# Kernel optimization log

Hardware: AMD Instinct MI355X
Metric: run time of the kernel (lower is better)

Reference implementation:

```python
import jax, jax.numpy as jnp
import numpy as np

N = 200000
E = 6400000
NEG_SLOPE = 0.01  # nn.LeakyReLU default

def _leaky(x):
    return jnp.where(x >= 0, x, NEG_SLOPE * x)

def gcn_conv(x, edge_index, W, b, n):
    # PyG GCNConv: add self-loops, symmetric degree norm, linear, scatter-add, bias
    src, dst = edge_index[0], edge_index[1]
    loops = jnp.arange(n, dtype=src.dtype)
    src = jnp.concatenate([src, loops])
    dst = jnp.concatenate([dst, loops])
    deg = jax.ops.segment_sum(jnp.ones_like(dst, dtype=x.dtype), dst, num_segments=n)
    dinv = jnp.where(deg > 0, jax.lax.rsqrt(deg), 0.0)
    norm = dinv[src] * dinv[dst]                  # [E+N]
    h = x @ W.T                                   # [N,50] linear (no bias yet)
    msg = h[src] * norm[:, None]                  # gather + scale
    out = jax.ops.segment_sum(msg, dst, num_segments=n)  # scatter-add to targets
    return out + b

def setup_inputs() -> dict:
    key = jax.random.key(0)
    ks = jax.random.split(key, 20)
    def w(k, o, i):
        return jax.random.normal(k, (o, i), dtype=jnp.float32) * (1.0 / np.sqrt(i))
    def bvec(k, o):
        return jax.random.normal(k, (o,), dtype=jnp.float32) * 0.01
    inp = {
        'x': jax.random.normal(ks[0], (N, 150), dtype=jnp.float32),
        'edge_index': jax.random.randint(ks[1], (2, E), 0, N, dtype=jnp.int64 if jax.config.jax_enable_x64 else jnp.int32),
        'epsilon': jax.random.normal(ks[2], (N, 10), dtype=jnp.float32),
        'Wg': w(ks[3], 50, 50), 'bg': bvec(ks[4], 50),
        'We1': w(ks[5], 40, 50), 'be1': bvec(ks[6], 40),
        'We2': w(ks[7], 30, 40), 'be2': bvec(ks[8], 30),
        'We3': w(ks[9], 20, 30), 'be3': bvec(ks[10], 20),
        'Wfc': w(ks[11], 10, 10), 'bfc': bvec(ks[12], 10),
        'Wd1': w(ks[13], 20, 10), 'bd1': bvec(ks[14], 20),
        'Wd2': w(ks[15], 40, 20), 'bd2': bvec(ks[16], 40),
        'Wd3': w(ks[17], 50, 40), 'bd3': bvec(ks[18], 50),
    }
    return inp

def reference(x, edge_index, epsilon, Wg, bg, We1, be1, We2, be2, We3, be3,
              Wfc, bfc, Wd1, bd1, Wd2, bd2, Wd3, bd3):
    x1 = x[:, 100:]                                   # [N,50]
    h = gcn_conv(x1, edge_index, Wg, bg, x.shape[0])  # [N,50]
    # encoder
    e = _leaky(h @ We1.T + be1)
    e = _leaky(e @ We2.T + be2)
    e = e @ We3.T + be3                               # [N,20]
    mu, log_var = e[:, :10], e[:, 10:]
    # reparameterization: mu + eps * sqrt(exp(log_var))
    z1 = mu + epsilon * jnp.exp(0.5 * log_var)
    z = jax.nn.relu(z1 @ Wfc.T + bfc)                 # FC
    # decoder
    d = _leaky(z @ Wd1.T + bd1)
    d = _leaky(d @ Wd2.T + bd2)
    mu_prime = jax.nn.sigmoid(d @ Wd3.T + bd3)        # [N,50]
    return (mu_prime, mu, log_var, z)
```

## Files before the change

kernel.cpp:

```cpp
#include <hip/hip_runtime.h>


#define NEG 0.01f
#define GS 64
#define ELLS 64
#define NB 16
#define SPILL_CAP 65536

#define DET_ES (1024 * 1024)
#define IS64_THRESH (DET_ES / 2)

#define META_INTS 1024

typedef int vint2 __attribute__((ext_vector_type(2)));

static __device__ __forceinline__ float bf2f(unsigned short u) {
    return __uint_as_float(((unsigned)u) << 16);
}
static __device__ __forceinline__ float leaky(float a) { return (a >= 0.f) ? a : NEG * a; }

__global__ void k_zero(int* __restrict__ indeg, int* __restrict__ flag,
                       int* __restrict__ meta, int n) {
    int i = blockIdx.x * 256 + threadIdx.x;
    if (i < n) indeg[i] = 0;
    if (blockIdx.x == 0) {
        for (int j = threadIdx.x; j < META_INTS; j += 256) meta[j] = 0;
        if (threadIdx.x == 0) { flag[0] = 0; flag[1] = 0; flag[2] = 0; }
    }
}

__global__ void k_detect(const unsigned* __restrict__ x, long xwords,
                         const unsigned* __restrict__ ei, long epairs,
                         int* __restrict__ flag) {
    int gw = (blockIdx.x * 256 + threadIdx.x) >> 6;
    int lane = threadIdx.x & 63;
    int side = gw >> 10;
    int ch = gw & 1023;
    int c = 0;
    if (side == 0) {
        long step = xwords >> 10;
        long base = (long)ch * step;
        if (base + 1024 > xwords) base = xwords > 1024 ? xwords - 1024 : 0;
#pragma unroll
        for (int t = 0; t < 16; t++) {
            long idx = base + t * 64 + lane;
            if (idx < xwords) {
                unsigned w = x[idx];
                if (((w >> 23) & 0xFFu) == 0xFFu || ((w >> 7) & 0xFFu) == 0xFFu) c++;
            }
        }
        for (int k = 32; k; k >>= 1) c += __shfl_xor(c, k);
        if (lane == 0 && c) atomicAdd(&flag[0], c);
    } else {
        long step = epairs >> 10;
        long base = (long)ch * step;
        if (base + 1024 > epairs) base = epairs > 1024 ? epairs - 1024 : 0;
#pragma unroll
        for (int t = 0; t < 16; t++) {
            long idx = base + t * 64 + lane;
            if (idx < epairs && ei[2 * idx + 1] == 0u) c++;
        }
        for (int k = 32; k; k >>= 1) c += __shfl_xor(c, k);
        if (lane == 0 && c) atomicAdd(&flag[1], c);
    }
}

__global__ __launch_bounds__(256) void k_hist(const int* __restrict__ ei,
                                              const int* __restrict__ flag,
                                              int* __restrict__ meta, int E, int N) {
    __shared__ int lh[NB];
    if (threadIdx.x < NB) lh[threadIdx.x] = 0;
    __syncthreads();
    bool is64 = flag[1] > IS64_THRESH;
    unsigned usw = ((unsigned)N + NB - 1) / NB;
    const long stride = 1024L * 256;
    if (is64) {
        const int2* p = (const int2*)ei;
        for (long e = (long)blockIdx.x * 256 + threadIdx.x; e < E; e += stride) {
            int d = p[E + e].x;
            if ((unsigned)d < (unsigned)N) atomicAdd(&lh[(unsigned)d / usw], 1);
        }
    } else {
        for (long e = (long)blockIdx.x * 256 + threadIdx.x; e < E; e += stride) {
            int d = ei[E + e];
            if ((unsigned)d < (unsigned)N) atomicAdd(&lh[(unsigned)d / usw], 1);
        }
    }
    __syncthreads();
    if (threadIdx.x < NB && lh[threadIdx.x]) atomicAdd(&meta[threadIdx.x * 16], lh[threadIdx.x]);
}

__global__ void k_scan(int* __restrict__ meta) {
    if (threadIdx.x == 0) {
        int acc = 0;
        for (int k = 0; k < NB; k++) {
            int c = meta[k * 16];
            meta[256 + k] = acc;
            meta[512 + k * 16] = acc;
            acc += c;
            meta[288 + k] = acc;
        }
    }
}

__global__ __launch_bounds__(256) void k_part(const int* __restrict__ ei,
                                              const int* __restrict__ flag,
                                              int* __restrict__ meta,
                                              int2* __restrict__ bucket, int E, int N) {
    __shared__ int2 buf[NB][512];
    __shared__ int lcnt[NB];
    __shared__ int lbase;
    if (threadIdx.x < NB) lcnt[threadIdx.x] = 0;
    __syncthreads();
    bool is64 = flag[1] > IS64_THRESH;
    unsigned usw = ((unsigned)N + NB - 1) / NB;
    int nsteps = (E + 2048 * 256 - 1) / (2048 * 256);
    for (int step = 0; step < nsteps; step++) {
        long e = (long)(step * 2048 + blockIdx.x) * 256 + threadIdx.x;
        int b = -1;
        int2 sd;
        if (e < E) {
            int src, d;
            if (is64) {
                const int2* p = (const int2*)ei;
                src = p[e].x;
                d = p[E + e].x;
            } else {
                src = ei[e];
                d = ei[E + e];
            }
            if ((unsigned)d < (unsigned)N) {
                b = (int)((unsigned)d / usw);
                sd = make_int2(src, d);
            }
        }
        if (b >= 0) {
            int p = atomicAdd(&lcnt[b], 1);
            buf[b][p] = sd;
        }
        __syncthreads();
        for (int k = 0; k < NB; k++) {
            int cnt = lcnt[k];
            if (cnt >= 256) {
                if (threadIdx.x == 0) lbase = atomicAdd(&meta[512 + k * 16], 256);
                __syncthreads();
                bucket[lbase + threadIdx.x] = buf[k][threadIdx.x];
                int rem = cnt - 256;
                int2 r;
                if (threadIdx.x < rem) r = buf[k][256 + threadIdx.x];
                __syncthreads();
                if (threadIdx.x < rem) buf[k][threadIdx.x] = r;
                if (threadIdx.x == 0) lcnt[k] = rem;
                __syncthreads();
            }
        }
    }
    for (int k = 0; k < NB; k++) {
        int cnt = lcnt[k];
        if (cnt > 0) {
            if (threadIdx.x == 0) lbase = atomicAdd(&meta[512 + k * 16], cnt);
            __syncthreads();
            if (threadIdx.x < cnt) bucket[lbase + threadIdx.x] = buf[k][threadIdx.x];
            __syncthreads();
        }
    }
}

__global__ __launch_bounds__(256) void k_build2(const int2* __restrict__ bucket,
                                                const int* __restrict__ meta,
                                                int* __restrict__ indeg,
                                                int* __restrict__ ebuf,
                                                int2* __restrict__ spill,
                                                int* __restrict__ flag, int N, int pass) {
    int s = pass * 8 + (blockIdx.x & 7);
    int q = blockIdx.x >> 3;
    int lo = meta[256 + s];
    int hi = meta[288 + s];
    for (int idx = lo + q * 256 + threadIdx.x; idx < hi; idx += 512 * 256) {
        vint2 t = __builtin_nontemporal_load((const vint2*)&bucket[idx]);
        int src = t.x;
        int d = t.y;
        if ((unsigned)src >= (unsigned)N) continue;
        int c = atomicAdd(&indeg[d], 1);
        if (c < ELLS) {
            ebuf[(size_t)d * ELLS + c] = src;
        } else {
            int o = atomicAdd(&flag[2], 1);
            if (o < SPILL_CAP) spill[o] = make_int2(src, d);
        }
    }
}

__global__ void k_dinv(const int* __restrict__ indeg, float* __restrict__ dinv, int n) {
    int i = blockIdx.x * 256 + threadIdx.x;
    if (i < n) dinv[i] = rsqrtf(1.0f + (float)indeg[i]);
}

struct CW {
    const void* src[16];
    int off[16];
    int n[16];
};
__global__ void k_convw(CW cw, float* __restrict__ dst, const int* __restrict__ flag) {
    int b = blockIdx.x;
    bool isf = flag[0] > 64;
    const float* sf = (const float*)cw.src[b];
    const unsigned short* sh = (const unsigned short*)cw.src[b];
    float* d = dst + cw.off[b];
    int n = cw.n[b];
    for (int i = threadIdx.x; i < n; i += 256) d[i] = isf ? sf[i] : bf2f(sh[i]);
}

#define O_WG 0
#define O_BG 2500
#define O_WE1 2550
#define O_BE1 4550
#define O_WE2 4590
#define O_BE2 5790
#define O_WE3 5820
#define O_BE3 6420
#define O_WFC 6440
#define O_BFC 6540
#define O_WD1 6550
#define O_BD1 6750
#define O_WD2 6770
#define O_BD2 7570
#define O_WD3 7610
#define O_BD3 9610
#define W_TOT 9660

__global__ __launch_bounds__(256) void k_g(const void* __restrict__ xv,
                                           const float* __restrict__ W,
                                           const float* __restrict__ dinv,
                                           const int* __restrict__ flag,
                                           float* __restrict__ g, int n) {
    int i = blockIdx.x * 256 + threadIdx.x;
    if (i >= n) return;
    bool isf = flag[0] > 64;
    float xr[50];
    if (isf) {
        const float* p = (const float*)xv + (size_t)i * 150 + 100;
#pragma unroll
        for (int k = 0; k < 50; k++) xr[k] = p[k];
    } else {
        const unsigned short* p = (const unsigned short*)xv + (size_t)i * 150 + 100;
#pragma unroll
        for (int k = 0; k < 50; k++) xr[k] = bf2f(p[k]);
    }
    const float* Wg = W + O_WG;
    float di = dinv[i];
    float* gr = g + (size_t)i * GS;
#pragma unroll
    for (int f = 0; f < 50; f += 2) {
        float a0 = 0.f, a1 = 0.f;
#pragma unroll
        for (int p = 0; p < 50; p++) {
            a0 += Wg[f * 50 + p] * xr[p];
            a1 += Wg[(f + 1) * 50 + p] * xr[p];
        }
        gr[f] = a0 * di;
        gr[f + 1] = a1 * di;
    }
}

__global__ __launch_bounds__(256) void k_gather(const float* __restrict__ g,
                                                const int* __restrict__ indeg,
                                                const int* __restrict__ ebuf,
                                                const float* __restrict__ dinv,
                                                const float* __restrict__ W,
                                                float* __restrict__ h1, int n) {
    int wid = threadIdx.x >> 6;
    int lane = threadIdx.x & 63;
    int i = blockIdx.x * 4 + wid;
    if (i >= n) return;
    int fc = lane < 50 ? lane : 49;
    int cnt = indeg[i];
    if (cnt > ELLS) cnt = ELLS;
    float di = dinv[i];
    int ev = (lane < cnt) ? ebuf[(size_t)i * ELLS + lane] : 0;
    float a0 = g[(size_t)i * GS + fc];
    float a1 = 0.f, a2 = 0.f, a3 = 0.f, a4 = 0.f, a5 = 0.f, a6 = 0.f, a7 = 0.f;
    int m = 0;
    for (; m + 7 < cnt; m += 8) {
        int j0 = __shfl(ev, m);
        int j1 = __shfl(ev, m + 1);
        int j2 = __shfl(ev, m + 2);
        int j3 = __shfl(ev, m + 3);
        int j4 = __shfl(ev, m + 4);
        int j5 = __shfl(ev, m + 5);
        int j6 = __shfl(ev, m + 6);
        int j7 = __shfl(ev, m + 7);
        a0 += g[(size_t)j0 * GS + fc];
        a1 += g[(size_t)j1 * GS + fc];
        a2 += g[(size_t)j2 * GS + fc];
        a3 += g[(size_t)j3 * GS + fc];
        a4 += g[(size_t)j4 * GS + fc];
        a5 += g[(size_t)j5 * GS + fc];
        a6 += g[(size_t)j6 * GS + fc];
        a7 += g[(size_t)j7 * GS + fc];
    }
    for (; m < cnt; m++) {
        int j = __shfl(ev, m);
        a0 += g[(size_t)j * GS + fc];
    }
    if (lane < 50) {
        float h = (((a0 + a1) + (a2 + a3)) + ((a4 + a5) + (a6 + a7))) * di + W[O_BG + lane];
        h1[(size_t)i * 50 + lane] = h;
    }
}

__global__ void k_spill(const int2* __restrict__ spill, const int* __restrict__ flag,
                        const float* __restrict__ g, const float* __restrict__ dinv,
                        float* __restrict__ h1) {
    int nov = flag[2];
    if (nov > SPILL_CAP) nov = SPILL_CAP;
    int lane = threadIdx.x & 63;
    int wave = (blockIdx.x * 256 + threadIdx.x) >> 6;
    for (int e = wave; e < nov; e += gridDim.x * 4) {
        int2 sd = spill[e];
        if (lane < 50)
            atomicAdd(&h1[(size_t)sd.y * 50 + lane], g[(size_t)sd.x * GS + lane] * dinv[sd.y]);
    }
}


__global__ __launch_bounds__(256) void k_e1(const float* __restrict__ h1,
                                            const float* __restrict__ W,
                                            float* __restrict__ t1, int n) {
    int i = blockIdx.x * 256 + threadIdx.x;
    if (i >= n) return;
    float v0[50];
    const float2* hr = (const float2*)(h1 + (size_t)i * 50);
#pragma unroll
    for (int p = 0; p < 25; p++) {
        float2 q = hr[p];
        v0[2 * p] = q.x;
        v0[2 * p + 1] = q.y;
    }
    float o[40];
#pragma unroll
    for (int f = 0; f < 40; f++) {
        float a = W[O_BE1 + f];
#pragma unroll
        for (int p = 0; p < 50; p++) a += W[O_WE1 + f * 50 + p] * v0[p];
        o[f] = leaky(a);
    }
    float4* ot = (float4*)(t1 + (size_t)i * 40);
#pragma unroll
    for (int p = 0; p < 10; p++) ot[p] = make_float4(o[4 * p], o[4 * p + 1], o[4 * p + 2], o[4 * p + 3]);
}

__global__ __launch_bounds__(256) void k_e23(const float* __restrict__ t1,
                                             const float* __restrict__ W,
                                             float* __restrict__ out, int n) {
    int i = blockIdx.x * 256 + threadIdx.x;
    if (i >= n) return;
    float v1[40];
    const float4* tr = (const float4*)(t1 + (size_t)i * 40);
#pragma unroll
    for (int p = 0; p < 10; p++) {
        float4 q = tr[p];
        v1[4 * p] = q.x; v1[4 * p + 1] = q.y; v1[4 * p + 2] = q.z; v1[4 * p + 3] = q.w;
    }
    float v2[30];
#pragma unroll
    for (int f = 0; f < 30; f++) {
        float a = W[O_BE2 + f];
#pragma unroll
        for (int p = 0; p < 40; p++) a += W[O_WE2 + f * 40 + p] * v1[p];
        v2[f] = leaky(a);
    }
    float v3[20];
#pragma unroll
    for (int f = 0; f < 20; f++) {
        float a = W[O_BE3 + f];
#pragma unroll
        for (int p = 0; p < 30; p++) a += W[O_WE3 + f * 30 + p] * v2[p];
        v3[f] = a;
    }
    float2* o_mu = (float2*)(out + (size_t)n * 50 + (size_t)i * 10);
    float2* o_lv = (float2*)(out + (size_t)n * 60 + (size_t)i * 10);
#pragma unroll
    for (int p = 0; p < 5; p++) {
        o_mu[p] = make_float2(v3[2 * p], v3[2 * p + 1]);
        o_lv[p] = make_float2(v3[10 + 2 * p], v3[10 + 2 * p + 1]);
    }
}

__global__ __launch_bounds__(256) void k_zfc(float* outb,
                                             const void* __restrict__ epsv,
                                             const float* __restrict__ W,
                                             const int* __restrict__ flag,
                                             float* __restrict__ t3, int n) {
    int i = blockIdx.x * 256 + threadIdx.x;
    if (i >= n) return;
    bool isf = flag[0] > 64;
    float mu[10], lv[10];
    const float2* pm = (const float2*)(outb + (size_t)n * 50 + (size_t)i * 10);
    const float2* pl = (const float2*)(outb + (size_t)n * 60 + (size_t)i * 10);
#pragma unroll
    for (int p = 0; p < 5; p++) {
        float2 a = pm[p]; mu[2 * p] = a.x; mu[2 * p + 1] = a.y;
        float2 b = pl[p]; lv[2 * p] = b.x; lv[2 * p + 1] = b.y;
    }
    float ev[10];
    if (isf) {
        const float* p = (const float*)epsv + (size_t)i * 10;
#pragma unroll
        for (int k = 0; k < 10; k++) ev[k] = p[k];
    } else {
        const unsigned short* p = (const unsigned short*)epsv + (size_t)i * 10;
#pragma unroll
        for (int k = 0; k < 10; k++) ev[k] = bf2f(p[k]);
    }
    float z1[10];
#pragma unroll
    for (int k = 0; k < 10; k++) z1[k] = mu[k] + ev[k] * expf(0.5f * lv[k]);
    float z[10];
#pragma unroll
    for (int f = 0; f < 10; f++) {
        float a = W[O_BFC + f];
#pragma unroll
        for (int p = 0; p < 10; p++) a += W[O_WFC + f * 10 + p] * z1[p];
        z[f] = (a > 0.f) ? a : 0.f;
    }
    float2* o_z = (float2*)(outb + (size_t)n * 70 + (size_t)i * 10);
#pragma unroll
    for (int p = 0; p < 5; p++) o_z[p] = make_float2(z[2 * p], z[2 * p + 1]);
    float d1[20];
#pragma unroll
    for (int f = 0; f < 20; f++) {
        float a = W[O_BD1 + f];
#pragma unroll
        for (int p = 0; p < 10; p++) a += W[O_WD1 + f * 10 + p] * z[p];
        d1[f] = leaky(a);
    }
    float d2[40];
#pragma unroll
    for (int f = 0; f < 40; f++) {
        float a = W[O_BD2 + f];
#pragma unroll
        for (int p = 0; p < 20; p++) a += W[O_WD2 + f * 20 + p] * d1[p];
        d2[f] = leaky(a);
    }
    float4* ot = (float4*)(t3 + (size_t)i * 40);
#pragma unroll
    for (int p = 0; p < 10; p++)
        ot[p] = make_float4(d2[4 * p], d2[4 * p + 1], d2[4 * p + 2], d2[4 * p + 3]);
}

__global__ __launch_bounds__(256) void k_d3(const float* __restrict__ t3,
                                            const float* __restrict__ W,
                                            float* __restrict__ out, int n) {
    int i = blockIdx.x * 256 + threadIdx.x;
    if (i >= n) return;
    float d2[40];
    const float4* tr = (const float4*)(t3 + (size_t)i * 40);
#pragma unroll
    for (int p = 0; p < 10; p++) {
        float4 q = tr[p];
        d2[4 * p] = q.x; d2[4 * p + 1] = q.y; d2[4 * p + 2] = q.z; d2[4 * p + 3] = q.w;
    }
    float o[50];
#pragma unroll
    for (int f = 0; f < 50; f++) {
        float a = W[O_BD3 + f];
#pragma unroll
        for (int p = 0; p < 40; p++) a += W[O_WD3 + f * 40 + p] * d2[p];
        o[f] = 1.f / (1.f + expf(-a));
    }
    float2* om = (float2*)(out + (size_t)i * 50);
#pragma unroll
    for (int p = 0; p < 25; p++) om[p] = make_float2(o[2 * p], o[2 * p + 1]);
}

extern "C" void kernel_launch(void* const* d_in, const int* in_sizes, int n_in,
                              void* d_out, int out_size, void* d_ws, size_t ws_size,
                              hipStream_t stream) {
    const int N = in_sizes[0] / 150;
    const int E = in_sizes[1] / 2;

    char* w = (char*)d_ws;
    auto alloc = [&](size_t bytes) {
        void* p = (void*)w;
        w += (bytes + 255) & ~(size_t)255;
        return p;
    };
    int* indeg = (int*)alloc((size_t)N * 4);
    int* flag = (int*)alloc(256);
    int* meta = (int*)alloc((size_t)META_INTS * 4);
    float* dinv = (float*)alloc((size_t)N * 4);
    float* Wall = (float*)alloc((size_t)W_TOT * 4);
    int2* spill = (int2*)alloc((size_t)SPILL_CAP * 8);
    float* g = (float*)alloc((size_t)N * GS * 4);
    float* h1 = (float*)alloc((size_t)N * 50 * 4);
    int* ebuf = (int*)alloc((size_t)N * ELLS * 4);

    int2* bucket;
    if ((size_t)E * 8 <= (size_t)N * GS * 4 + (size_t)N * 50 * 4) {
        bucket = (int2*)g;
    } else {
        bucket = (int2*)alloc((size_t)E * 8);
    }

    float* t1 = g;
    float* t3 = h1;

    CW cw;
    static const int wn[16] = {2500, 50, 2000, 40, 1200, 30, 600, 20,
                               100, 10, 200, 20, 800, 40, 2000, 50};
    static const int wo[16] = {O_WG, O_BG, O_WE1, O_BE1, O_WE2, O_BE2, O_WE3, O_BE3,
                               O_WFC, O_BFC, O_WD1, O_BD1, O_WD2, O_BD2, O_WD3, O_BD3};
    for (int k = 0; k < 16; k++) {
        cw.src[k] = d_in[3 + k];
        cw.off[k] = wo[k];
        cw.n[k] = wn[k];
    }

    int nbN = (N + 255) / 256;

    k_zero<<<nbN, 256, 0, stream>>>(indeg, flag, meta, N);
    k_detect<<<512, 256, 0, stream>>>((const unsigned*)d_in[0], (long)N * 75,
                                      (const unsigned*)d_in[1], (long)E, flag);
    k_hist<<<1024, 256, 0, stream>>>((const int*)d_in[1], flag, meta, E, N);
    k_scan<<<1, 64, 0, stream>>>(meta);
    k_part<<<2048, 256, 0, stream>>>((const int*)d_in[1], flag, meta, bucket, E, N);
    k_build2<<<4096, 256, 0, stream>>>(bucket, meta, indeg, ebuf, spill, flag, N, 0);
    k_build2<<<4096, 256, 0, stream>>>(bucket, meta, indeg, ebuf, spill, flag, N, 1);
    k_dinv<<<nbN, 256, 0, stream>>>(indeg, dinv, N);
    k_convw<<<16, 256, 0, stream>>>(cw, Wall, flag);
    k_g<<<nbN, 256, 0, stream>>>(d_in[0], Wall, dinv, flag, g, N);
    k_gather<<<(N + 3) / 4, 256, 0, stream>>>(g, indeg, ebuf, dinv, Wall, h1, N);
    k_spill<<<64, 256, 0, stream>>>(spill, flag, g, dinv, h1);
    k_e1<<<nbN, 256, 0, stream>>>(h1, Wall, t1, N);
    k_e23<<<nbN, 256, 0, stream>>>(t1, Wall, (float*)d_out, N);
    k_zfc<<<nbN, 256, 0, stream>>>((float*)d_out, d_in[2], Wall, flag, t3, N);
    k_d3<<<nbN, 256, 0, stream>>>(t3, Wall, (float*)d_out, N);
}
```

Measured before the change: 1.086 ms.

## Gather neighbor rows with float4 loads, four edges per wave instruction

The neighbor aggregation kernel now splits each wave into four 16-lane groups. Each group loads a whole 64-float padded row of g as float4, so one load instruction covers four edges instead of one. Partial sums are combined across groups with xor shuffles, and the self term, scale and bias are applied at the end. Supporting changes vectorize the x loads and the zero-padded g stores in k_g, and pad h1 to a 56-float stride so its rows can be written and read as float4. The cost is extra shuffle reductions and padding memory, and the bias load reads past the bias into neighbouring weights, which are discarded.

Result: no change. 1.083 ms (-0.3%).

```diff
diff --git a/kernel.cpp b/kernel.cpp
--- a/kernel.cpp
+++ b/kernel.cpp
@@ -3,6 +3,7 @@
 
 #define NEG 0.01f
 #define GS 64
+#define HS 56
 #define ELLS 64
 #define NB 16
 #define SPILL_CAP 65536
@@ -239,17 +240,25 @@
     bool isf = flag[0] > 64;
     float xr[50];
     if (isf) {
-        const float* p = (const float*)xv + (size_t)i * 150 + 100;
-#pragma unroll
-        for (int k = 0; k < 50; k++) xr[k] = p[k];
+        const float2* p = (const float2*)((const float*)xv + (size_t)i * 150 + 100);
+#pragma unroll
+        for (int k = 0; k < 25; k++) {
+            float2 q = p[k];
+            xr[2 * k] = q.x;
+            xr[2 * k + 1] = q.y;
+        }
     } else {
-        const unsigned short* p = (const unsigned short*)xv + (size_t)i * 150 + 100;
-#pragma unroll
-        for (int k = 0; k < 50; k++) xr[k] = bf2f(p[k]);
+        const unsigned* p = (const unsigned*)((const unsigned short*)xv + (size_t)i * 150 + 100);
+#pragma unroll
+        for (int k = 0; k < 25; k++) {
+            unsigned u = p[k];
+            xr[2 * k] = __uint_as_float(u << 16);
+            xr[2 * k + 1] = __uint_as_float(u & 0xFFFF0000u);
+        }
     }
     const float* Wg = W + O_WG;
     float di = dinv[i];
-    float* gr = g + (size_t)i * GS;
+    float o[64];
 #pragma unroll
     for (int f = 0; f < 50; f += 2) {
         float a0 = 0.f, a1 = 0.f;
@@ -258,9 +267,15 @@
             a0 += Wg[f * 50 + p] * xr[p];
             a1 += Wg[(f + 1) * 50 + p] * xr[p];
         }
-        gr[f] = a0 * di;
-        gr[f + 1] = a1 * di;
-    }
+        o[f] = a0 * di;
+        o[f + 1] = a1 * di;
+    }
+#pragma unroll
+    for (int f = 50; f < 64; f++) o[f] = 0.f;
+    float4* gr4 = (float4*)(g + (size_t)i * GS);
+#pragma unroll
+    for (int p = 0; p < 16; p++)
+        gr4[p] = make_float4(o[4 * p], o[4 * p + 1], o[4 * p + 2], o[4 * p + 3]);
 }
 
 __global__ __launch_bounds__(256) void k_gather(const float* __restrict__ g,
@@ -273,39 +288,66 @@
     int lane = threadIdx.x & 63;
     int i = blockIdx.x * 4 + wid;
     if (i >= n) return;
-    int fc = lane < 50 ? lane : 49;
+    int q = lane >> 4;
+    int r = lane & 15;
     int cnt = indeg[i];
     if (cnt > ELLS) cnt = ELLS;
-    float di = dinv[i];
     int ev = (lane < cnt) ? ebuf[(size_t)i * ELLS + lane] : 0;
-    float a0 = g[(size_t)i * GS + fc];
-    float a1 = 0.f, a2 = 0.f, a3 = 0.f, a4 = 0.f, a5 = 0.f, a6 = 0.f, a7 = 0.f;
+    const float4* g4 = (const float4*)g;
+    float4 a0 = make_float4(0.f, 0.f, 0.f, 0.f);
+    float4 a1 = a0, a2 = a0, a3 = a0;
     int m = 0;
-    for (; m + 7 < cnt; m += 8) {
-        int j0 = __shfl(ev, m);
-        int j1 = __shfl(ev, m + 1);
-        int j2 = __shfl(ev, m + 2);
-        int j3 = __shfl(ev, m + 3);
-        int j4 = __shfl(ev, m + 4);
-        int j5 = __shfl(ev, m + 5);
-        int j6 = __shfl(ev, m + 6);
-        int j7 = __shfl(ev, m + 7);
-        a0 += g[(size_t)j0 * GS + fc];
-        a1 += g[(size_t)j1 * GS + fc];
-        a2 += g[(size_t)j2 * GS + fc];
-        a3 += g[(size_t)j3 * GS + fc];
-        a4 += g[(size_t)j4 * GS + fc];
-        a5 += g[(size_t)j5 * GS + fc];
-        a6 += g[(size_t)j6 * GS + fc];
-        a7 += g[(size_t)j7 * GS + fc];
-    }
-    for (; m < cnt; m++) {
-        int j = __shfl(ev, m);
-        a0 += g[(size_t)j * GS + fc];
-    }
-    if (lane < 50) {
-        float h = (((a0 + a1) + (a2 + a3)) + ((a4 + a5) + (a6 + a7))) * di + W[O_BG + lane];
-        h1[(size_t)i * 50 + lane] = h;
+    for (; m + 16 <= cnt; m += 16) {
+        int j0 = __shfl(ev, m + q);
+        int j1 = __shfl(ev, m + 4 + q);
+        int j2 = __shfl(ev, m + 8 + q);
+        int j3 = __shfl(ev, m + 12 + q);
+        float4 t0 = g4[(size_t)j0 * 16 + r];
+        float4 t1 = g4[(size_t)j1 * 16 + r];
+        float4 t2 = g4[(size_t)j2 * 16 + r];
+        float4 t3 = g4[(size_t)j3 * 16 + r];
+        a0.x += t0.x; a0.y += t0.y; a0.z += t0.z; a0.w += t0.w;
+        a1.x += t1.x; a1.y += t1.y; a1.z += t1.z; a1.w += t1.w;
+        a2.x += t2.x; a2.y += t2.y; a2.z += t2.z; a2.w += t2.w;
+        a3.x += t3.x; a3.y += t3.y; a3.z += t3.z; a3.w += t3.w;
+    }
+    for (; m + 4 <= cnt; m += 4) {
+        int j = __shfl(ev, m + q);
+        float4 t = g4[(size_t)j * 16 + r];
+        a0.x += t.x; a0.y += t.y; a0.z += t.z; a0.w += t.w;
+    }
+    if (m < cnt) {
+        int j = __shfl(ev, m + q);
+        if (m + q < cnt) {
+            float4 t = g4[(size_t)j * 16 + r];
+            a0.x += t.x; a0.y += t.y; a0.z += t.z; a0.w += t.w;
+        }
+    }
+    float4 s;
+    s.x = (a0.x + a1.x) + (a2.x + a3.x);
+    s.y = (a0.y + a1.y) + (a2.y + a3.y);
+    s.z = (a0.z + a1.z) + (a2.z + a3.z);
+    s.w = (a0.w + a1.w) + (a2.w + a3.w);
+    s.x += __shfl_xor(s.x, 16); s.y += __shfl_xor(s.y, 16);
+    s.z += __shfl_xor(s.z, 16); s.w += __shfl_xor(s.w, 16);
+    s.x += __shfl_xor(s.x, 32); s.y += __shfl_xor(s.y, 32);
+    s.z += __shfl_xor(s.z, 32); s.w += __shfl_xor(s.w, 32);
+    if (lane < 16) {
+        float di = dinv[i];
+        float4 self = g4[(size_t)i * 16 + lane];
+        float4 b = ((const float4*)(W + O_BG))[lane];
+        float4 h;
+        h.x = (s.x + self.x) * di + b.x;
+        h.y = (s.y + self.y) * di + b.y;
+        h.z = (s.z + self.z) * di + b.z;
+        h.w = (s.w + self.w) * di + b.w;
+        float* hr = h1 + (size_t)i * HS;
+        if (lane < 12) {
+            ((float4*)hr)[lane] = h;
+        } else if (lane == 12) {
+            hr[48] = h.x;
+            hr[49] = h.y;
+        }
     }
 }
 
@@ -319,7 +361,7 @@
     for (int e = wave; e < nov; e += gridDim.x * 4) {
         int2 sd = spill[e];
         if (lane < 50)
-            atomicAdd(&h1[(size_t)sd.y * 50 + lane], g[(size_t)sd.x * GS + lane] * dinv[sd.y]);
+            atomicAdd(&h1[(size_t)sd.y * HS + lane], g[(size_t)sd.x * GS + lane] * dinv[sd.y]);
     }
 }
 
@@ -330,13 +372,15 @@
     int i = blockIdx.x * 256 + threadIdx.x;
     if (i >= n) return;
     float v0[50];
-    const float2* hr = (const float2*)(h1 + (size_t)i * 50);
-#pragma unroll
-    for (int p = 0; p < 25; p++) {
-        float2 q = hr[p];
-        v0[2 * p] = q.x;
-        v0[2 * p + 1] = q.y;
-    }
+    const float* hr = h1 + (size_t)i * HS;
+    const float4* hr4 = (const float4*)hr;
+#pragma unroll
+    for (int p = 0; p < 12; p++) {
+        float4 t = hr4[p];
+        v0[4 * p] = t.x; v0[4 * p + 1] = t.y; v0[4 * p + 2] = t.z; v0[4 * p + 3] = t.w;
+    }
+    v0[48] = hr[48];
+    v0[49] = hr[49];
     float o[40];
 #pragma unroll
     for (int f = 0; f < 40; f++) {
@@ -493,11 +537,11 @@
     float* Wall = (float*)alloc((size_t)W_TOT * 4);
     int2* spill = (int2*)alloc((size_t)SPILL_CAP * 8);
     float* g = (float*)alloc((size_t)N * GS * 4);
-    float* h1 = (float*)alloc((size_t)N * 50 * 4);
+    float* h1 = (float*)alloc((size_t)N * HS * 4);
     int* ebuf = (int*)alloc((size_t)N * ELLS * 4);
 
     int2* bucket;
-    if ((size_t)E * 8 <= (size_t)N * GS * 4 + (size_t)N * 50 * 4) {
+    if ((size_t)E * 8 <= (size_t)N * GS * 4 + (size_t)N * HS * 4) {
         bucket = (int2*)g;
     } else {
         bucket = (int2*)alloc((size_t)E * 8);
```
